# Performance work log

Hardware: AMD Instinct MI355X
Metric: run time of the kernel (lower is better)

Reference implementation:

```python
import jax, jax.numpy as jnp
import numpy as np

B, C, M, N = 8, 64, 256, 256
THRESHOLD = 0.8
EPS = 1e-5
PAD = 3  # kernel_size=7


def conv2d(x, w, b=None):
    # x: (B,Cin,H,W), w: (Cout,Cin,7,7), stride 1, 'same' padding 3
    y = jax.lax.conv_general_dilated(
        x, w, window_strides=(1, 1), padding=[(PAD, PAD), (PAD, PAD)],
        dimension_numbers=('NCHW', 'OIHW', 'NCHW'))
    if b is not None:
        y = y + b[None, :, None, None]
    return y


def region_norm(region, mask):
    # region: (B,C,M,N) zeroed outside region; mask: (B,C,M,N) binary
    s = jnp.sum(region, axis=(0, 2, 3))            # (C,)
    Sr = jnp.sum(mask, axis=(0, 2, 3))             # (C,)
    Sr = jnp.where(Sr == 0, 1.0, Sr)
    mu = (s / Sr)[None, :, None, None]
    t = region + (1.0 - mask) * mu                 # fill surroundings with region mean
    # BatchNorm2d(affine=False, track_running_stats=False): batch stats, biased var
    m = jnp.mean(t, axis=(0, 2, 3), keepdims=True)
    v = jnp.mean((t - m) ** 2, axis=(0, 2, 3), keepdims=True)
    bn = (t - m) * jax.lax.rsqrt(v + EPS)
    scale = jnp.sqrt(Sr / (region.shape[0] * region.shape[2] * region.shape[3]))
    return bn * scale[None, :, None, None]


def setup_inputs() -> dict:
    key = jax.random.key(0)
    k = jax.random.split(key, 6)
    x = jax.random.normal(k[0], (B, C, M, N), dtype=jnp.float32)
    # conv1: Conv2d(2,1,7,bias=False); gamma/beta: Conv2d(1,1,7) with bias
    w1 = jax.random.normal(k[1], (1, 2, 7, 7), dtype=jnp.float32) * 0.1
    wg = jax.random.normal(k[2], (1, 1, 7, 7), dtype=jnp.float32) * 0.1
    bg = jax.random.normal(k[3], (1,), dtype=jnp.float32) * 0.1
    wb = jax.random.normal(k[4], (1, 1, 7, 7), dtype=jnp.float32) * 0.1
    bb = jax.random.normal(k[5], (1,), dtype=jnp.float32) * 0.1
    return {"x": x, "w1": w1, "wg": wg, "bg": bg, "wb": wb, "bb": bb}


def reference(x, w1, wg, bg, wb, bb):
    # SelfAware_Affine
    avg_out = jnp.mean(x, axis=1, keepdims=True)       # (B,1,M,N)
    max_out = jnp.max(x, axis=1, keepdims=True)        # (B,1,M,N)
    sa_in = jnp.concatenate([avg_out, max_out], axis=1)
    sa_map = jax.nn.sigmoid(conv2d(sa_in, w1))         # (B,1,M,N)
    gamma = conv2d(sa_map, wg, bg)                     # (B,1,M,N)
    beta = conv2d(sa_map, wb, bb)                      # (B,1,M,N)
    # binary mask from detached importance map, expanded over channels
    mask = (jax.lax.stop_gradient(sa_map) >= THRESHOLD).astype(x.dtype)
    mask = jnp.broadcast_to(mask, x.shape)             # (B,C,M,N)
    rn_x = region_norm(x * mask, mask) + region_norm(x * (1.0 - mask), 1.0 - mask)
    return rn_x * (1.0 + gamma) + beta
```

## Files before the change

### kernel.cpp

```cpp
#include <hip/hip_runtime.h>
#include <cmath>

#define B_ 8
#define C_ 64
#define M_ 256
#define N_ 256
#define PLANE_ (M_*N_)
#define PIX_ (B_*PLANE_)
#define THRESH_ 0.8f
#define EPS_ 1e-5f

__global__ void k_avgmax(const float* __restrict__ x,
                         float* __restrict__ avgp, float* __restrict__ maxp,
                         float* __restrict__ acc) {
    if (blockIdx.x == 0) {
        if (threadIdx.x < 4 * C_) acc[threadIdx.x] = 0.f;
        if (threadIdx.x == 0) acc[4 * C_] = 0.f;
    }
    int idx4 = (blockIdx.x * blockDim.x + threadIdx.x) * 4;
    int b = idx4 >> 16;
    int p = idx4 & (PLANE_ - 1);
    const float* xb = x + (size_t)b * C_ * PLANE_ + p;
    float4 s = make_float4(0.f, 0.f, 0.f, 0.f);
    float4 mx = make_float4(-INFINITY, -INFINITY, -INFINITY, -INFINITY);
    #pragma unroll 8
    for (int c = 0; c < C_; ++c) {
        float4 v = *(const float4*)(xb + (size_t)c * PLANE_);
        s.x += v.x; s.y += v.y; s.z += v.z; s.w += v.w;
        mx.x = fmaxf(mx.x, v.x); mx.y = fmaxf(mx.y, v.y);
        mx.z = fmaxf(mx.z, v.z); mx.w = fmaxf(mx.w, v.w);
    }
    const float r = 1.f / C_;
    s.x *= r; s.y *= r; s.z *= r; s.w *= r;
    *(float4*)(avgp + idx4) = s;
    *(float4*)(maxp + idx4) = mx;
}

#define TW_ 64
#define TH_ 16
#define SAW_ (TW_+6)
#define SAH_ (TH_+6)
#define LDW_ (TW_+12)
#define LDH_ (TH_+12)

__global__ void k_sa_fused(const float* __restrict__ avgp, const float* __restrict__ maxp,
                           const float* __restrict__ w1,
                           const float* __restrict__ wg, const float* __restrict__ bgp,
                           const float* __restrict__ wb, const float* __restrict__ bbp,
                           float* __restrict__ gammap, float* __restrict__ betap,
                           unsigned char* __restrict__ maskp, int* __restrict__ cntp) {
    __shared__ float sA[LDH_][LDW_];
    __shared__ float sM[LDH_][LDW_];
    __shared__ float sSA[SAH_][SAW_];
    __shared__ float w[196];
    __shared__ int bcnt;
    int tid = threadIdx.x;
    if (tid < 98) w[tid] = w1[tid];
    else if (tid < 196) w[tid] = (tid < 147) ? wg[tid - 98] : wb[tid - 147];
    if (tid == 196) bcnt = 0;

    int tileid = blockIdx.x;
    int b = blockIdx.y;
    int ti0 = (tileid >> 2) * TH_;
    int tj0 = (tileid & 3) * TW_;
    const float* a = avgp + (size_t)b * PLANE_;
    const float* m = maxp + (size_t)b * PLANE_;

    for (int idx = tid; idx < LDH_ * LDW_; idx += 256) {
        int li = idx / LDW_;
        int lj = idx - li * LDW_;
        int gi = ti0 - 6 + li, gj = tj0 - 6 + lj;
        bool ok = ((unsigned)gi < (unsigned)M_) && ((unsigned)gj < (unsigned)N_);
        int o = gi * N_ + gj;
        sA[li][lj] = ok ? a[o] : 0.f;
        sM[li][lj] = ok ? m[o] : 0.f;
    }
    __syncthreads();

    for (int idx = tid; idx < SAH_ * SAW_; idx += 256) {
        int si = idx / SAW_;
        int sj = idx - si * SAW_;
        int gi = ti0 - 3 + si, gj = tj0 - 3 + sj;
        float v = 0.f;
        if ((unsigned)gi < (unsigned)M_ && (unsigned)gj < (unsigned)N_) {
            float acc = 0.f;
            #pragma unroll
            for (int dh = 0; dh < 7; ++dh) {
                #pragma unroll
                for (int dw = 0; dw < 7; ++dw) {
                    acc += sA[si + dh][sj + dw] * w[dh * 7 + dw]
                         + sM[si + dh][sj + dw] * w[49 + dh * 7 + dw];
                }
            }
            v = 1.f / (1.f + expf(-acc));
        }
        sSA[si][sj] = v;
    }
    __syncthreads();

    float bgv = bgp[0], bbv = bbp[0];
    int lcnt = 0;
    #pragma unroll
    for (int k = 0; k < 4; ++k) {
        int p = k * 256 + tid;
        int ti = p >> 6, tj = p & 63;
        float g = 0.f, be = 0.f;
        #pragma unroll
        for (int dh = 0; dh < 7; ++dh) {
            #pragma unroll
            for (int dw = 0; dw < 7; ++dw) {
                float v = sSA[ti + dh][tj + dw];
                g  += v * w[98 + dh * 7 + dw];
                be += v * w[147 + dh * 7 + dw];
            }
        }
        int idx = b * PLANE_ + (ti0 + ti) * N_ + (tj0 + tj);
        gammap[idx] = g + bgv;
        betap[idx]  = be + bbv;
        int mk = (sSA[ti + 3][tj + 3] >= THRESH_) ? 1 : 0;
        maskp[idx] = (unsigned char)mk;
        lcnt += mk;
    }
    for (int off = 32; off > 0; off >>= 1) lcnt += __shfl_down(lcnt, off, 64);
    if ((tid & 63) == 0) atomicAdd(&bcnt, lcnt);
    __syncthreads();
    if (tid == 0) atomicAdd(cntp, bcnt);
}

__global__ void k_sums(const float* __restrict__ x, const unsigned char* __restrict__ maskp,
                       float* __restrict__ S, float* __restrict__ Q,
                       float* __restrict__ S1, float* __restrict__ Q1) {
    int chunk = blockIdx.x;
    int c = blockIdx.y;
    int b = blockIdx.z;
    const float* xp = x + ((size_t)(b * C_ + c)) * PLANE_ + chunk * 8192;
    const unsigned char* mp = maskp + (size_t)b * PLANE_ + chunk * 8192;
    float s = 0.f, q = 0.f, s1 = 0.f, q1 = 0.f;
    #pragma unroll
    for (int k = 0; k < 8; ++k) {
        int t = (k * 256 + threadIdx.x) * 4;
        float4 v = *(const float4*)(xp + t);
        uchar4 mm = *(const uchar4*)(mp + t);
        float m0 = (float)mm.x, m1 = (float)mm.y, m2 = (float)mm.z, m3 = (float)mm.w;
        s  += v.x + v.y + v.z + v.w;
        q  += v.x * v.x + v.y * v.y + v.z * v.z + v.w * v.w;
        s1 += v.x * m0 + v.y * m1 + v.z * m2 + v.w * m3;
        q1 += v.x * v.x * m0 + v.y * v.y * m1 + v.z * v.z * m2 + v.w * v.w * m3;
    }
    for (int off = 32; off > 0; off >>= 1) {
        s  += __shfl_down(s, off, 64);
        q  += __shfl_down(q, off, 64);
        s1 += __shfl_down(s1, off, 64);
        q1 += __shfl_down(q1, off, 64);
    }
    __shared__ float ls[4][4];
    int wave = threadIdx.x >> 6, lane = threadIdx.x & 63;
    if (lane == 0) { ls[wave][0] = s; ls[wave][1] = q; ls[wave][2] = s1; ls[wave][3] = q1; }
    __syncthreads();
    if (threadIdx.x == 0) {
        float ts = 0.f, tq = 0.f, ts1 = 0.f, tq1 = 0.f;
        #pragma unroll
        for (int wv = 0; wv < 4; ++wv) { ts += ls[wv][0]; tq += ls[wv][1]; ts1 += ls[wv][2]; tq1 += ls[wv][3]; }
        atomicAdd(&S[c], ts); atomicAdd(&Q[c], tq);
        atomicAdd(&S1[c], ts1); atomicAdd(&Q1[c], tq1);
    }
}

__global__ void k_final(const float* __restrict__ x, const unsigned char* __restrict__ maskp,
                        const float* __restrict__ gammap, const float* __restrict__ betap,
                        const float* __restrict__ S, const float* __restrict__ Q,
                        const float* __restrict__ S1, const float* __restrict__ Q1,
                        const int* __restrict__ cntp,
                        float* __restrict__ out) {
    int c = blockIdx.y;
    int b = blockIdx.z;
    const float P = (float)PIX_;
    int cnt1 = *cntp;
    float fc1 = (float)cnt1;
    float fc0 = P - fc1;
    float Sr1 = (cnt1 == 0) ? 1.f : fc1;
    float Sr0 = (cnt1 == PIX_) ? 1.f : fc0;
    float Sv = S[c], Qv = Q[c], S1v = S1[c], Q1v = Q1[c];
    float S0v = Sv - S1v, Q0v = Qv - Q1v;
    float mu1 = S1v / Sr1;
    float mu0 = S0v / Sr0;
    float m1 = (S1v + fc0 * mu1) / P;
    float v1 = fmaxf((Q1v + fc0 * mu1 * mu1) / P - m1 * m1, 0.f);
    float m0 = (S0v + fc1 * mu0) / P;
    float v0 = fmaxf((Q0v + fc1 * mu0 * mu0) / P - m0 * m0, 0.f);
    float A1 = rsqrtf(v1 + EPS_) * sqrtf(Sr1 / P);
    float A0 = rsqrtf(v0 + EPS_) * sqrtf(Sr0 / P);
    float B1 = (mu1 - m1) * A1;
    float B0 = (mu0 - m0) * A0;
    float ma = A1, mb = -m1 * A1 + B0;
    float ua = A0, ub = -m0 * A0 + B1;

    int p0 = blockIdx.x * 1024 + threadIdx.x * 4;
    size_t base = ((size_t)(b * C_ + c)) * PLANE_ + p0;
    int pp = b * PLANE_ + p0;
    float4 xv = *(const float4*)(x + base);
    float4 gv = *(const float4*)(gammap + pp);
    float4 bv = *(const float4*)(betap + pp);
    uchar4 mv = *(const uchar4*)(maskp + pp);
    float4 o;
    o.x = (mv.x ? xv.x * ma + mb : xv.x * ua + ub) * (1.f + gv.x) + bv.x;
    o.y = (mv.y ? xv.y * ma + mb : xv.y * ua + ub) * (1.f + gv.y) + bv.y;
    o.z = (mv.z ? xv.z * ma + mb : xv.z * ua + ub) * (1.f + gv.z) + bv.z;
    o.w = (mv.w ? xv.w * ma + mb : xv.w * ua + ub) * (1.f + gv.w) + bv.w;
    *(float4*)(out + base) = o;
}

extern "C" void kernel_launch(void* const* d_in, const int* in_sizes, int n_in,
                              void* d_out, int out_size, void* d_ws, size_t ws_size,
                              hipStream_t stream) {
    const float* x  = (const float*)d_in[0];
    const float* w1 = (const float*)d_in[1];
    const float* wg = (const float*)d_in[2];
    const float* bg = (const float*)d_in[3];
    const float* wb = (const float*)d_in[4];
    const float* bb = (const float*)d_in[5];
    float* out = (float*)d_out;

    float* ws = (float*)d_ws;
    float* avgp   = ws;
    float* maxp   = avgp + PIX_;
    float* gammap = maxp + PIX_;
    float* betap  = gammap + PIX_;
    float* S   = betap + PIX_;
    float* Q   = S + C_;
    float* S1  = Q + C_;
    float* Q1  = S1 + C_;
    int*   cnt = (int*)(Q1 + C_);
    unsigned char* maskp = (unsigned char*)(cnt + 1);

    k_avgmax<<<PIX_ / (256 * 4), 256, 0, stream>>>(x, avgp, maxp, S);
    dim3 g2(64, B_);
    k_sa_fused<<<g2, 256, 0, stream>>>(avgp, maxp, w1, wg, bg, wb, bb,
                                       gammap, betap, maskp, cnt);
    dim3 g3(8, C_, B_);
    k_sums<<<g3, 256, 0, stream>>>(x, maskp, S, Q, S1, Q1);
    dim3 g5(PLANE_ / 1024, C_, B_);
    k_final<<<g5, 256, 0, stream>>>(x, maskp, gammap, betap, S, Q, S1, Q1, cnt, out);
}
```

Before: 335.5 us.

## Fuse four kernels into one cooperative persistent kernel with grid syncs

Result: slower. 652.4 us (+94.5%).

```diff
diff --git a/kernel.cpp b/kernel.cpp
--- a/kernel.cpp
+++ b/kernel.cpp
@@ -1,5 +1,8 @@
 #include <hip/hip_runtime.h>
+#include <hip/hip_cooperative_groups.h>
 #include <cmath>
+
+namespace cg = cooperative_groups;
 
 #define B_ 8
 #define C_ 64
@@ -10,204 +13,215 @@
 #define THRESH_ 0.8f
 #define EPS_ 1e-5f
 
-__global__ void k_avgmax(const float* __restrict__ x,
-                         float* __restrict__ avgp, float* __restrict__ maxp,
-                         float* __restrict__ acc) {
-    if (blockIdx.x == 0) {
-        if (threadIdx.x < 4 * C_) acc[threadIdx.x] = 0.f;
-        if (threadIdx.x == 0) acc[4 * C_] = 0.f;
-    }
-    int idx4 = (blockIdx.x * blockDim.x + threadIdx.x) * 4;
-    int b = idx4 >> 16;
-    int p = idx4 & (PLANE_ - 1);
-    const float* xb = x + (size_t)b * C_ * PLANE_ + p;
-    float4 s = make_float4(0.f, 0.f, 0.f, 0.f);
-    float4 mx = make_float4(-INFINITY, -INFINITY, -INFINITY, -INFINITY);
-    #pragma unroll 8
-    for (int c = 0; c < C_; ++c) {
-        float4 v = *(const float4*)(xb + (size_t)c * PLANE_);
-        s.x += v.x; s.y += v.y; s.z += v.z; s.w += v.w;
-        mx.x = fmaxf(mx.x, v.x); mx.y = fmaxf(mx.y, v.y);
-        mx.z = fmaxf(mx.z, v.z); mx.w = fmaxf(mx.w, v.w);
-    }
-    const float r = 1.f / C_;
-    s.x *= r; s.y *= r; s.z *= r; s.w *= r;
-    *(float4*)(avgp + idx4) = s;
-    *(float4*)(maxp + idx4) = mx;
-}
-
 #define TW_ 64
 #define TH_ 16
 #define SAW_ (TW_+6)
 #define SAH_ (TH_+6)
 #define LDW_ (TW_+12)
 #define LDH_ (TH_+12)
-
-__global__ void k_sa_fused(const float* __restrict__ avgp, const float* __restrict__ maxp,
-                           const float* __restrict__ w1,
-                           const float* __restrict__ wg, const float* __restrict__ bgp,
-                           const float* __restrict__ wb, const float* __restrict__ bbp,
-                           float* __restrict__ gammap, float* __restrict__ betap,
-                           unsigned char* __restrict__ maskp, int* __restrict__ cntp) {
+#define NTILES_ (64 * B_)
+
+__global__ __launch_bounds__(256, 4)
+void k_mega(const float* __restrict__ x, const float* __restrict__ w1,
+            const float* __restrict__ wg, const float* __restrict__ bgp,
+            const float* __restrict__ wb, const float* __restrict__ bbp,
+            float* __restrict__ avgp, float* __restrict__ maxp,
+            float* __restrict__ gammap, float* __restrict__ betap,
+            float* __restrict__ acc, unsigned char* __restrict__ maskp,
+            float* __restrict__ out) {
+    cg::grid_group grid = cg::this_grid();
+    const int tid = threadIdx.x;
+    const int bid = blockIdx.x;
+    const int nb  = gridDim.x;
+    float* S  = acc;
+    float* Q  = acc + C_;
+    float* S1 = acc + 2 * C_;
+    float* Q1 = acc + 3 * C_;
+    int* cntp = (int*)(acc + 4 * C_);
+
     __shared__ float sA[LDH_][LDW_];
     __shared__ float sM[LDH_][LDW_];
     __shared__ float sSA[SAH_][SAW_];
     __shared__ float w[196];
+    __shared__ float ls[4][4];
     __shared__ int bcnt;
-    int tid = threadIdx.x;
+
+    if (bid == 0) {
+        if (tid < 4 * C_) acc[tid] = 0.f;
+        if (tid == 0) acc[4 * C_] = 0.f;
+    }
+    for (int g = bid * 256 + tid; g < PIX_ / 4; g += nb * 256) {
+        int idx4 = g * 4;
+        int b = idx4 >> 16;
+        int p = idx4 & (PLANE_ - 1);
+        const float* xb = x + (size_t)b * C_ * PLANE_ + p;
+        float4 s = make_float4(0.f, 0.f, 0.f, 0.f);
+        float4 mx = make_float4(-INFINITY, -INFINITY, -INFINITY, -INFINITY);
+        #pragma unroll 8
+        for (int c = 0; c < C_; ++c) {
+            float4 v = *(const float4*)(xb + (size_t)c * PLANE_);
+            s.x += v.x; s.y += v.y; s.z += v.z; s.w += v.w;
+            mx.x = fmaxf(mx.x, v.x); mx.y = fmaxf(mx.y, v.y);
+            mx.z = fmaxf(mx.z, v.z); mx.w = fmaxf(mx.w, v.w);
+        }
+        const float r = 1.f / C_;
+        s.x *= r; s.y *= r; s.z *= r; s.w *= r;
+        *(float4*)(avgp + idx4) = s;
+        *(float4*)(maxp + idx4) = mx;
+    }
+    __threadfence();
+    grid.sync();
+
     if (tid < 98) w[tid] = w1[tid];
     else if (tid < 196) w[tid] = (tid < 147) ? wg[tid - 98] : wb[tid - 147];
-    if (tid == 196) bcnt = 0;
-
-    int tileid = blockIdx.x;
-    int b = blockIdx.y;
-    int ti0 = (tileid >> 2) * TH_;
-    int tj0 = (tileid & 3) * TW_;
-    const float* a = avgp + (size_t)b * PLANE_;
-    const float* m = maxp + (size_t)b * PLANE_;
-
-    for (int idx = tid; idx < LDH_ * LDW_; idx += 256) {
-        int li = idx / LDW_;
-        int lj = idx - li * LDW_;
-        int gi = ti0 - 6 + li, gj = tj0 - 6 + lj;
-        bool ok = ((unsigned)gi < (unsigned)M_) && ((unsigned)gj < (unsigned)N_);
-        int o = gi * N_ + gj;
-        sA[li][lj] = ok ? a[o] : 0.f;
-        sM[li][lj] = ok ? m[o] : 0.f;
-    }
-    __syncthreads();
-
-    for (int idx = tid; idx < SAH_ * SAW_; idx += 256) {
-        int si = idx / SAW_;
-        int sj = idx - si * SAW_;
-        int gi = ti0 - 3 + si, gj = tj0 - 3 + sj;
-        float v = 0.f;
-        if ((unsigned)gi < (unsigned)M_ && (unsigned)gj < (unsigned)N_) {
-            float acc = 0.f;
+    float bgv = bgp[0], bbv = bbp[0];
+    for (int tile = bid; tile < NTILES_; tile += nb) {
+        __syncthreads();
+        if (tid == 0) bcnt = 0;
+        int b = tile >> 6;
+        int t = tile & 63;
+        int ti0 = (t >> 2) * TH_;
+        int tj0 = (t & 3) * TW_;
+        const float* a = avgp + (size_t)b * PLANE_;
+        const float* m = maxp + (size_t)b * PLANE_;
+        for (int idx = tid; idx < LDH_ * LDW_; idx += 256) {
+            int li = idx / LDW_;
+            int lj = idx - li * LDW_;
+            int gi = ti0 - 6 + li, gj = tj0 - 6 + lj;
+            bool ok = ((unsigned)gi < (unsigned)M_) && ((unsigned)gj < (unsigned)N_);
+            int o = gi * N_ + gj;
+            sA[li][lj] = ok ? a[o] : 0.f;
+            sM[li][lj] = ok ? m[o] : 0.f;
+        }
+        __syncthreads();
+        for (int idx = tid; idx < SAH_ * SAW_; idx += 256) {
+            int si = idx / SAW_;
+            int sj = idx - si * SAW_;
+            int gi = ti0 - 3 + si, gj = tj0 - 3 + sj;
+            float v = 0.f;
+            if ((unsigned)gi < (unsigned)M_ && (unsigned)gj < (unsigned)N_) {
+                float a2 = 0.f;
+                #pragma unroll
+                for (int dh = 0; dh < 7; ++dh)
+                    #pragma unroll
+                    for (int dw = 0; dw < 7; ++dw)
+                        a2 += sA[si + dh][sj + dw] * w[dh * 7 + dw]
+                            + sM[si + dh][sj + dw] * w[49 + dh * 7 + dw];
+                v = 1.f / (1.f + expf(-a2));
+            }
+            sSA[si][sj] = v;
+        }
+        __syncthreads();
+        int lcnt = 0;
+        #pragma unroll
+        for (int k = 0; k < 4; ++k) {
+            int p = k * 256 + tid;
+            int ti = p >> 6, tj = p & 63;
+            float g = 0.f, be = 0.f;
             #pragma unroll
-            for (int dh = 0; dh < 7; ++dh) {
+            for (int dh = 0; dh < 7; ++dh)
                 #pragma unroll
                 for (int dw = 0; dw < 7; ++dw) {
-                    acc += sA[si + dh][sj + dw] * w[dh * 7 + dw]
-                         + sM[si + dh][sj + dw] * w[49 + dh * 7 + dw];
+                    float v = sSA[ti + dh][tj + dw];
+                    g  += v * w[98 + dh * 7 + dw];
+                    be += v * w[147 + dh * 7 + dw];
                 }
-            }
-            v = 1.f / (1.f + expf(-acc));
-        }
-        sSA[si][sj] = v;
-    }
-    __syncthreads();
-
-    float bgv = bgp[0], bbv = bbp[0];
-    int lcnt = 0;
-    #pragma unroll
-    for (int k = 0; k < 4; ++k) {
-        int p = k * 256 + tid;
-        int ti = p >> 6, tj = p & 63;
-        float g = 0.f, be = 0.f;
+            int idx = b * PLANE_ + (ti0 + ti) * N_ + (tj0 + tj);
+            gammap[idx] = g + bgv;
+            betap[idx]  = be + bbv;
+            int mk = (sSA[ti + 3][tj + 3] >= THRESH_) ? 1 : 0;
+            maskp[idx] = (unsigned char)mk;
+            lcnt += mk;
+        }
+        for (int off = 32; off > 0; off >>= 1) lcnt += __shfl_down(lcnt, off, 64);
+        if ((tid & 63) == 0) atomicAdd(&bcnt, lcnt);
+        __syncthreads();
+        if (tid == 0) atomicAdd(cntp, bcnt);
+    }
+    __threadfence();
+    grid.sync();
+
+    for (int it = bid; it < 8 * C_ * B_; it += nb) {
+        int chunk = it & 7;
+        int c = (it >> 3) & 63;
+        int b = it >> 9;
+        const float* xp = x + ((size_t)(b * C_ + c)) * PLANE_ + chunk * 8192;
+        const unsigned char* mp = maskp + (size_t)b * PLANE_ + chunk * 8192;
+        float s = 0.f, q = 0.f, s1 = 0.f, q1 = 0.f;
         #pragma unroll
-        for (int dh = 0; dh < 7; ++dh) {
+        for (int k = 0; k < 8; ++k) {
+            int t = (k * 256 + tid) * 4;
+            float4 v = *(const float4*)(xp + t);
+            uchar4 mm = *(const uchar4*)(mp + t);
+            float m0 = (float)mm.x, m1 = (float)mm.y, m2 = (float)mm.z, m3 = (float)mm.w;
+            s  += v.x + v.y + v.z + v.w;
+            q  += v.x * v.x + v.y * v.y + v.z * v.z + v.w * v.w;
+            s1 += v.x * m0 + v.y * m1 + v.z * m2 + v.w * m3;
+            q1 += v.x * v.x * m0 + v.y * v.y * m1 + v.z * v.z * m2 + v.w * v.w * m3;
+        }
+        for (int off = 32; off > 0; off >>= 1) {
+            s  += __shfl_down(s, off, 64);
+            q  += __shfl_down(q, off, 64);
+            s1 += __shfl_down(s1, off, 64);
+            q1 += __shfl_down(q1, off, 64);
+        }
+        int wave = tid >> 6, lane = tid & 63;
+        if (lane == 0) { ls[wave][0] = s; ls[wave][1] = q; ls[wave][2] = s1; ls[wave][3] = q1; }
+        __syncthreads();
+        if (tid == 0) {
+            float ts = 0.f, tq = 0.f, ts1 = 0.f, tq1 = 0.f;
             #pragma unroll
-            for (int dw = 0; dw < 7; ++dw) {
-                float v = sSA[ti + dh][tj + dw];
-                g  += v * w[98 + dh * 7 + dw];
-                be += v * w[147 + dh * 7 + dw];
-            }
-        }
-        int idx = b * PLANE_ + (ti0 + ti) * N_ + (tj0 + tj);
-        gammap[idx] = g + bgv;
-        betap[idx]  = be + bbv;
-        int mk = (sSA[ti + 3][tj + 3] >= THRESH_) ? 1 : 0;
-        maskp[idx] = (unsigned char)mk;
-        lcnt += mk;
-    }
-    for (int off = 32; off > 0; off >>= 1) lcnt += __shfl_down(lcnt, off, 64);
-    if ((tid & 63) == 0) atomicAdd(&bcnt, lcnt);
-    __syncthreads();
-    if (tid == 0) atomicAdd(cntp, bcnt);
-}
-
-__global__ void k_sums(const float* __restrict__ x, const unsigned char* __restrict__ maskp,
-                       float* __restrict__ S, float* __restrict__ Q,
-                       float* __restrict__ S1, float* __restrict__ Q1) {
-    int chunk = blockIdx.x;
-    int c = blockIdx.y;
-    int b = blockIdx.z;
-    const float* xp = x + ((size_t)(b * C_ + c)) * PLANE_ + chunk * 8192;
-    const unsigned char* mp = maskp + (size_t)b * PLANE_ + chunk * 8192;
-    float s = 0.f, q = 0.f, s1 = 0.f, q1 = 0.f;
-    #pragma unroll
-    for (int k = 0; k < 8; ++k) {
-        int t = (k * 256 + threadIdx.x) * 4;
-        float4 v = *(const float4*)(xp + t);
-        uchar4 mm = *(const uchar4*)(mp + t);
-        float m0 = (float)mm.x, m1 = (float)mm.y, m2 = (float)mm.z, m3 = (float)mm.w;
-        s  += v.x + v.y + v.z + v.w;
-        q  += v.x * v.x + v.y * v.y + v.z * v.z + v.w * v.w;
-        s1 += v.x * m0 + v.y * m1 + v.z * m2 + v.w * m3;
-        q1 += v.x * v.x * m0 + v.y * v.y * m1 + v.z * v.z * m2 + v.w * v.w * m3;
-    }
-    for (int off = 32; off > 0; off >>= 1) {
-        s  += __shfl_down(s, off, 64);
-        q  += __shfl_down(q, off, 64);
-        s1 += __shfl_down(s1, off, 64);
-        q1 += __shfl_down(q1, off, 64);
-    }
-    __shared__ float ls[4][4];
-    int wave = threadIdx.x >> 6, lane = threadIdx.x & 63;
-    if (lane == 0) { ls[wave][0] = s; ls[wave][1] = q; ls[wave][2] = s1; ls[wave][3] = q1; }
-    __syncthreads();
-    if (threadIdx.x == 0) {
-        float ts = 0.f, tq = 0.f, ts1 = 0.f, tq1 = 0.f;
-        #pragma unroll
-        for (int wv = 0; wv < 4; ++wv) { ts += ls[wv][0]; tq += ls[wv][1]; ts1 += ls[wv][2]; tq1 += ls[wv][3]; }
-        atomicAdd(&S[c], ts); atomicAdd(&Q[c], tq);
-        atomicAdd(&S1[c], ts1); atomicAdd(&Q1[c], tq1);
-    }
-}
-
-__global__ void k_final(const float* __restrict__ x, const unsigned char* __restrict__ maskp,
-                        const float* __restrict__ gammap, const float* __restrict__ betap,
-                        const float* __restrict__ S, const float* __restrict__ Q,
-                        const float* __restrict__ S1, const float* __restrict__ Q1,
-                        const int* __restrict__ cntp,
-                        float* __restrict__ out) {
-    int c = blockIdx.y;
-    int b = blockIdx.z;
+            for (int wv = 0; wv < 4; ++wv) { ts += ls[wv][0]; tq += ls[wv][1]; ts1 += ls[wv][2]; tq1 += ls[wv][3]; }
+            atomicAdd(&S[c], ts); atomicAdd(&Q[c], tq);
+            atomicAdd(&S1[c], ts1); atomicAdd(&Q1[c], tq1);
+        }
+        __syncthreads();
+    }
+    __threadfence();
+    grid.sync();
+
     const float P = (float)PIX_;
     int cnt1 = *cntp;
     float fc1 = (float)cnt1;
     float fc0 = P - fc1;
     float Sr1 = (cnt1 == 0) ? 1.f : fc1;
     float Sr0 = (cnt1 == PIX_) ? 1.f : fc0;
-    float Sv = S[c], Qv = Q[c], S1v = S1[c], Q1v = Q1[c];
-    float S0v = Sv - S1v, Q0v = Qv - Q1v;
-    float mu1 = S1v / Sr1;
-    float mu0 = S0v / Sr0;
-    float m1 = (S1v + fc0 * mu1) / P;
-    float v1 = fmaxf((Q1v + fc0 * mu1 * mu1) / P - m1 * m1, 0.f);
-    float m0 = (S0v + fc1 * mu0) / P;
-    float v0 = fmaxf((Q0v + fc1 * mu0 * mu0) / P - m0 * m0, 0.f);
-    float A1 = rsqrtf(v1 + EPS_) * sqrtf(Sr1 / P);
-    float A0 = rsqrtf(v0 + EPS_) * sqrtf(Sr0 / P);
-    float B1 = (mu1 - m1) * A1;
-    float B0 = (mu0 - m0) * A0;
-    float ma = A1, mb = -m1 * A1 + B0;
-    float ua = A0, ub = -m0 * A0 + B1;
-
-    int p0 = blockIdx.x * 1024 + threadIdx.x * 4;
-    size_t base = ((size_t)(b * C_ + c)) * PLANE_ + p0;
-    int pp = b * PLANE_ + p0;
-    float4 xv = *(const float4*)(x + base);
-    float4 gv = *(const float4*)(gammap + pp);
-    float4 bv = *(const float4*)(betap + pp);
-    uchar4 mv = *(const uchar4*)(maskp + pp);
-    float4 o;
-    o.x = (mv.x ? xv.x * ma + mb : xv.x * ua + ub) * (1.f + gv.x) + bv.x;
-    o.y = (mv.y ? xv.y * ma + mb : xv.y * ua + ub) * (1.f + gv.y) + bv.y;
-    o.z = (mv.z ? xv.z * ma + mb : xv.z * ua + ub) * (1.f + gv.z) + bv.z;
-    o.w = (mv.w ? xv.w * ma + mb : xv.w * ua + ub) * (1.f + gv.w) + bv.w;
-    *(float4*)(out + base) = o;
+    float sq1 = sqrtf(Sr1 / P), sq0 = sqrtf(Sr0 / P);
+    for (int it = bid; it < 8 * C_ * B_; it += nb) {
+        int chunk = it & 7;
+        int c = (it >> 3) & 63;
+        int b = it >> 9;
+        float Sv = S[c], Qv = Q[c], S1v = S1[c], Q1v = Q1[c];
+        float S0v = Sv - S1v, Q0v = Qv - Q1v;
+        float mu1 = S1v / Sr1;
+        float mu0 = S0v / Sr0;
+        float m1 = (S1v + fc0 * mu1) / P;
+        float v1 = fmaxf((Q1v + fc0 * mu1 * mu1) / P - m1 * m1, 0.f);
+        float m0 = (S0v + fc1 * mu0) / P;
+        float v0 = fmaxf((Q0v + fc1 * mu0 * mu0) / P - m0 * m0, 0.f);
+        float A1 = rsqrtf(v1 + EPS_) * sq1;
+        float A0 = rsqrtf(v0 + EPS_) * sq0;
+        float B1 = (mu1 - m1) * A1;
+        float B0 = (mu0 - m0) * A0;
+        float ma = A1, mb = -m1 * A1 + B0;
+        float ua = A0, ub = -m0 * A0 + B1;
+        size_t cbase = ((size_t)(b * C_ + c)) * PLANE_ + chunk * 8192;
+        int pbase = b * PLANE_ + chunk * 8192;
+        #pragma unroll
+        for (int k = 0; k < 8; ++k) {
+            int t = (k * 256 + tid) * 4;
+            float4 xv = *(const float4*)(x + cbase + t);
+            float4 gv = *(const float4*)(gammap + pbase + t);
+            float4 bv = *(const float4*)(betap + pbase + t);
+            uchar4 mv = *(const uchar4*)(maskp + pbase + t);
+            float4 o;
+            o.x = (mv.x ? xv.x * ma + mb : xv.x * ua + ub) * (1.f + gv.x) + bv.x;
+            o.y = (mv.y ? xv.y * ma + mb : xv.y * ua + ub) * (1.f + gv.y) + bv.y;
+            o.z = (mv.z ? xv.z * ma + mb : xv.z * ua + ub) * (1.f + gv.z) + bv.z;
+            o.w = (mv.w ? xv.w * ma + mb : xv.w * ua + ub) * (1.f + gv.w) + bv.w;
+            *(float4*)(out + cbase + t) = o;
+        }
+    }
 }
 
 extern "C" void kernel_launch(void* const* d_in, const int* in_sizes, int n_in,
@@ -226,19 +240,35 @@
     float* maxp   = avgp + PIX_;
     float* gammap = maxp + PIX_;
     float* betap  = gammap + PIX_;
-    float* S   = betap + PIX_;
-    float* Q   = S + C_;
-    float* S1  = Q + C_;
-    float* Q1  = S1 + C_;
-    int*   cnt = (int*)(Q1 + C_);
-    unsigned char* maskp = (unsigned char*)(cnt + 1);
-
-    k_avgmax<<<PIX_ / (256 * 4), 256, 0, stream>>>(x, avgp, maxp, S);
-    dim3 g2(64, B_);
-    k_sa_fused<<<g2, 256, 0, stream>>>(avgp, maxp, w1, wg, bg, wb, bb,
-                                       gammap, betap, maskp, cnt);
-    dim3 g3(8, C_, B_);
-    k_sums<<<g3, 256, 0, stream>>>(x, maskp, S, Q, S1, Q1);
-    dim3 g5(PLANE_ / 1024, C_, B_);
-    k_final<<<g5, 256, 0, stream>>>(x, maskp, gammap, betap, S, Q, S1, Q1, cnt, out);
+    float* acc    = betap + PIX_;
+    unsigned char* maskp = (unsigned char*)(acc + 4 * C_ + 1);
+
+    static int gridBlocks = 0;
+    if (gridBlocks == 0) {
+        int bpc = 0;
+        hipError_t e = hipOccupancyMaxActiveBlocksPerMultiprocessor(
+            &bpc, (const void*)k_mega, 256, 0);
+        if (e != hipSuccess || bpc < 1) bpc = 2;
+        long g = (long)bpc * 256;
+        if (g > 1024) g = 1024;
+        if (g < 256) g = 256;
+        gridBlocks = (int)g;
+    }
+
+    void* args[13];
+    args[0]  = (void*)&x;
+    args[1]  = (void*)&w1;
+    args[2]  = (void*)&wg;
+    args[3]  = (void*)&bg;
+    args[4]  = (void*)&wb;
+    args[5]  = (void*)&bb;
+    args[6]  = (void*)&avgp;
+    args[7]  = (void*)&maxp;
+    args[8]  = (void*)&gammap;
+    args[9]  = (void*)&betap;
+    args[10] = (void*)&acc;
+    args[11] = (void*)&maskp;
+    args[12] = (void*)&out;
+    hipLaunchCooperativeKernel((const void*)k_mega, dim3(gridBlocks), dim3(256),
+                               args, 0, stream);
 }
```
